# Kernel optimization log

Hardware: AMD Instinct MI355X
Metric: run time of the kernel (lower is better)

## Reference

```python
import jax, jax.numpy as jnp
import numpy as np

B, D = 64, 512          # batch, in_dims
P, PS, S = 128, 3, 64   # num_patches, patch_size, scene_size


def setup_inputs() -> dict:
    key = jax.random.key(0)
    k0, k1, k2, k3 = jax.random.split(key, 4)
    z = jax.random.normal(k0, (B, D), jnp.float32)
    Wm = jax.random.normal(k1, (P * PS * PS, D), jnp.float32) * 0.02
    bm = jnp.zeros((P * PS * PS,), jnp.float32)
    Wt = jax.random.normal(k2, (6 * P, D), jnp.float32) * 0.01
    # module initializes transform bias to [scale,0,0,0,scale,0] per patch (scale=2)
    bt = jnp.tile(jnp.array([2.0, 0.0, 0.0, 0.0, 2.0, 0.0], jnp.float32), P)
    noise = jax.random.normal(k3, (PS, PS), jnp.float32)
    return {"z": z, "Wm": Wm, "bm": bm, "Wt": Wt, "bt": bt, "noise": noise}


def _affine_grid(theta, size):
    # theta: (N,2,3). Matches torch affine_grid(align_corners=False).
    c = (jnp.arange(size, dtype=theta.dtype) + 0.5) / size * 2.0 - 1.0
    xg, yg = jnp.meshgrid(c, c)  # xg[h,w]=c[w], yg[h,w]=c[h]
    base = jnp.stack([xg, yg, jnp.ones_like(xg)], axis=-1)  # (S,S,3)
    return jnp.einsum('nij,hwj->nhwi', theta, base)  # (N,S,S,2), [...,0]=x, [...,1]=y


def _grid_sample_bilinear_zeros(img, grid):
    # img: (N,Hi,Wi), grid: (N,Ho,Wo,2). torch grid_sample bilinear, zeros padding,
    # align_corners=False.
    N, Hi, Wi = img.shape
    ix = ((grid[..., 0] + 1.0) * Wi - 1.0) * 0.5
    iy = ((grid[..., 1] + 1.0) * Hi - 1.0) * 0.5
    ix0 = jnp.floor(ix)
    iy0 = jnp.floor(iy)
    wx1 = ix - ix0
    wy1 = iy - iy0
    wx0 = 1.0 - wx1
    wy0 = 1.0 - wy1
    b = jnp.arange(N)[:, None, None]

    def gather(xf, yf):
        xi = xf.astype(jnp.int32)
        yi = yf.astype(jnp.int32)
        valid = (xi >= 0) & (xi < Wi) & (yi >= 0) & (yi < Hi)
        xc = jnp.clip(xi, 0, Wi - 1)
        yc = jnp.clip(yi, 0, Hi - 1)
        return jnp.where(valid, img[b, yc, xc], 0.0)

    v00 = gather(ix0, iy0)
    v01 = gather(ix0 + 1.0, iy0)
    v10 = gather(ix0, iy0 + 1.0)
    v11 = gather(ix0 + 1.0, iy0 + 1.0)
    return (wy0 * (wx0 * v00 + wx1 * v01) + wy1 * (wx0 * v10 + wx1 * v11))


def reference(z, Wm, bm, Wt, bt, noise):
    Bz = z.shape[0]
    # refine_patches=True path: masks = 1 - sigmoid(Linear(z))
    masks = 1.0 - jax.nn.sigmoid(z @ Wm.T + bm)
    masks = masks.reshape(Bz, P, PS, PS) * noise  # patch_noise multiply
    theta = (z @ Wt.T + bt).reshape(Bz, P, 2, 3)
    imgs = masks.reshape(Bz * P, PS, PS)
    th = theta.reshape(Bz * P, 2, 3)
    grid = _affine_grid(th, S)                      # (B*P, S, S, 2)
    out = _grid_sample_bilinear_zeros(imgs, grid)   # (B*P, S, S)
    return out.reshape(Bz, P, S, S)
```

## Files before the change

### kernel.cpp

```cpp
#include <hip/hip_runtime.h>
#include <math.h>

#define BATCH 64
#define DIM 512
#define NPATCH 128
#define SSZ 64
#define NMASK 1152
#define NTHETA 768
#define NROWS 1920

__global__ __launch_bounds__(256) void k1_gemm(
    const float* __restrict__ z, const float* __restrict__ Wm,
    const float* __restrict__ bm, const float* __restrict__ Wt,
    const float* __restrict__ bt, const float* __restrict__ noise,
    float* __restrict__ tmp) {
  __shared__ float zs[64][65];
  __shared__ float ws[16][64];

  const int t = threadIdx.x;
  const int rowBase = blockIdx.x * 16;
  const int b = t & 63;
  const int rgrp = t >> 6;

  float acc0 = 0.f, acc1 = 0.f, acc2 = 0.f, acc3 = 0.f;

  const int zb = t >> 2, zseg = t & 3;
  const int wrow = t >> 4, wseg = t & 15;
  const int j_w = rowBase + wrow;
  const float* wsrc = (j_w < NMASK) ? (Wm + (size_t)j_w * DIM)
                                    : (Wt + (size_t)(j_w - NMASK) * DIM);

  for (int kc = 0; kc < DIM; kc += 64) {
    __syncthreads();
    {
      const float4* zsrc4 = (const float4*)(z + (size_t)zb * DIM + kc + zseg * 16);
      float* zd = &zs[zb][zseg * 16];
#pragma unroll
      for (int u = 0; u < 4; ++u) {
        float4 a = zsrc4[u];
        zd[u * 4 + 0] = a.x; zd[u * 4 + 1] = a.y;
        zd[u * 4 + 2] = a.z; zd[u * 4 + 3] = a.w;
      }
    }
    {
      float4 wv = *(const float4*)(wsrc + kc + wseg * 4);
      *(float4*)&ws[wrow][wseg * 4] = wv;
    }
    __syncthreads();
#pragma unroll 8
    for (int k = 0; k < 64; ++k) {
      float zv = zs[b][k];
      acc0 = fmaf(zv, ws[rgrp * 4 + 0][k], acc0);
      acc1 = fmaf(zv, ws[rgrp * 4 + 1][k], acc1);
      acc2 = fmaf(zv, ws[rgrp * 4 + 2][k], acc2);
      acc3 = fmaf(zv, ws[rgrp * 4 + 3][k], acc3);
    }
  }

  float accs[4] = {acc0, acc1, acc2, acc3};
#pragma unroll
  for (int rr = 0; rr < 4; ++rr) {
    int j = rowBase + rgrp * 4 + rr;
    float v = accs[rr];
    if (j < NMASK) {
      v = 1.0f / (1.0f + expf(v + bm[j]));
      v *= noise[j % 9];
    } else {
      v += bt[j - NMASK];
    }
    tmp[(size_t)j * 64 + b] = v;
  }
}

__global__ __launch_bounds__(256) void k2_sample(
    const float* __restrict__ tmp, float* __restrict__ out) {
  __shared__ float msp[56];
  __shared__ float ths[6];

  const int t = threadIdx.x;
  const int bp = blockIdx.x;
  const int b = bp >> 7;
  const int p = bp & 127;

  if (t < 56) {
    int r = t >> 3, c = t & 7;
    float v = 0.0f;
    if (r >= 2 && r <= 4 && c >= 2 && c <= 4) {
      int q = (r - 2) * 3 + (c - 2);
      v = tmp[(size_t)(p * 9 + q) * 64 + b];
    }
    msp[t] = v;
  } else if (t < 62) {
    ths[t - 56] = tmp[(size_t)(NMASK + p * 6 + (t - 56)) * 64 + b];
  }
  __syncthreads();

  const float th0 = ths[0], th1 = ths[1], th2 = ths[2];
  const float th3 = ths[3], th4 = ths[4], th5 = ths[5];

  const int w = t & 63;
  const float cx = (w + 0.5f) * (1.0f / 32.0f) - 1.0f;
  const float A  = fmaf(1.5f, fmaf(th0, cx, th2), 1.0f);
  const float Bx = 1.5f * th1;
  const float C  = fmaf(1.5f, fmaf(th3, cx, th5), 1.0f);
  const float By = 1.5f * th4;

  float* obase = out + ((size_t)bp << 12) + t;
  const int h0 = t >> 6;

#pragma unroll
  for (int i = 0; i < 16; ++i) {
    const int h = h0 + i * 4;
    const float cy = (h + 0.5f) * (1.0f / 32.0f) - 1.0f;
    float ix = fmaf(Bx, cy, A);
    float iy = fmaf(By, cy, C);
    ix = fminf(fmaxf(ix, -1.5f), 3.5f);
    iy = fminf(fmaxf(iy, -1.5f), 3.5f);
    float fx0 = floorf(ix);
    float fy0 = floorf(iy);
    float fx = ix - fx0;
    float fy = iy - fy0;
    int xi = (int)fx0;
    int yi = (int)fy0;
    int idx = (yi + 2) * 8 + (xi + 2);
    float v00 = msp[idx];
    float v01 = msp[idx + 1];
    float v10 = msp[idx + 8];
    float v11 = msp[idx + 9];
    float wx0 = 1.0f - fx;
    float t0 = fmaf(fx, v01, wx0 * v00);
    float t1 = fmaf(fx, v11, wx0 * v10);
    float r  = fmaf(fy, t1, (1.0f - fy) * t0);
    obase[(size_t)i * 256] = r;
  }
}

extern "C" void kernel_launch(void* const* d_in, const int* in_sizes, int n_in,
                              void* d_out, int out_size, void* d_ws, size_t ws_size,
                              hipStream_t stream) {
  const float* z     = (const float*)d_in[0];
  const float* Wm    = (const float*)d_in[1];
  const float* bm    = (const float*)d_in[2];
  const float* Wt    = (const float*)d_in[3];
  const float* bt    = (const float*)d_in[4];
  const float* noise = (const float*)d_in[5];
  float* out = (float*)d_out;
  float* tmp = (float*)d_ws;

  hipLaunchKernelGGL(k1_gemm, dim3(NROWS / 16), dim3(256), 0, stream,
                     z, Wm, bm, Wt, bt, noise, tmp);
  hipLaunchKernelGGL(k2_sample, dim3(BATCH * NPATCH), dim3(256), 0, stream,
                     tmp, out);
}
```

Measured before the change: 164.2 us.

## Use tent-weight bilinear sampling with float4 stores in sample kernel

Replaces the floor-and-gather bilinear lookup from a padded shared-memory patch with a closed-form tent-weight sum over the nine patch values held in registers. Each thread now computes four adjacent output pixels incrementally and writes them with a single float4 store. The aim is to remove the dynamic LDS indexing, floor and int conversion, and to widen global stores. In exchange each pixel costs more ALU work (six weights and a 3x3 weighted sum), and the incremental coordinate updates may round slightly differently from the original.

```diff
diff --git a/kernel.cpp b/kernel.cpp
--- a/kernel.cpp
+++ b/kernel.cpp
@@ -74,64 +74,61 @@
 
 __global__ __launch_bounds__(256) void k2_sample(
     const float* __restrict__ tmp, float* __restrict__ out) {
-  __shared__ float msp[56];
-  __shared__ float ths[6];
+  __shared__ float sm[15];
 
   const int t = threadIdx.x;
   const int bp = blockIdx.x;
   const int b = bp >> 7;
   const int p = bp & 127;
 
-  if (t < 56) {
-    int r = t >> 3, c = t & 7;
-    float v = 0.0f;
-    if (r >= 2 && r <= 4 && c >= 2 && c <= 4) {
-      int q = (r - 2) * 3 + (c - 2);
-      v = tmp[(size_t)(p * 9 + q) * 64 + b];
-    }
-    msp[t] = v;
-  } else if (t < 62) {
-    ths[t - 56] = tmp[(size_t)(NMASK + p * 6 + (t - 56)) * 64 + b];
+  if (t < 9) {
+    sm[t] = tmp[(size_t)(p * 9 + t) * 64 + b];
+  } else if (t < 15) {
+    sm[t] = tmp[(size_t)(NMASK + p * 6 + (t - 9)) * 64 + b];
   }
   __syncthreads();
 
-  const float th0 = ths[0], th1 = ths[1], th2 = ths[2];
-  const float th3 = ths[3], th4 = ths[4], th5 = ths[5];
+  const float m00 = sm[0], m01 = sm[1], m02 = sm[2];
+  const float m10 = sm[3], m11 = sm[4], m12 = sm[5];
+  const float m20 = sm[6], m21 = sm[7], m22 = sm[8];
+  const float th0 = sm[9], th1 = sm[10], th2 = sm[11];
+  const float th3 = sm[12], th4 = sm[13], th5 = sm[14];
 
-  const int w = t & 63;
-  const float cx = (w + 0.5f) * (1.0f / 32.0f) - 1.0f;
-  const float A  = fmaf(1.5f, fmaf(th0, cx, th2), 1.0f);
-  const float Bx = 1.5f * th1;
-  const float C  = fmaf(1.5f, fmaf(th3, cx, th5), 1.0f);
-  const float By = 1.5f * th4;
+  const int w4 = (t & 15) << 2;
+  const int hb = t >> 4;
+  const float cx0 = (w4 + 0.5f) * (1.0f / 32.0f) - 1.0f;
+  const float cy0 = (hb + 0.5f) * (1.0f / 32.0f) - 1.0f;
+  const float dix = th0 * (1.5f / 32.0f);
+  const float diy = th3 * (1.5f / 32.0f);
+  const float Bx = 1.5f * th1, By = 1.5f * th4;
+  const float Px = fmaf(1.5f, fmaf(th0, cx0, th2), 1.0f);
+  const float Py = fmaf(1.5f, fmaf(th3, cx0, th5), 1.0f);
 
-  float* obase = out + ((size_t)bp << 12) + t;
-  const int h0 = t >> 6;
+  float* op = out + ((size_t)bp << 12) + hb * 64 + w4;
 
 #pragma unroll
-  for (int i = 0; i < 16; ++i) {
-    const int h = h0 + i * 4;
-    const float cy = (h + 0.5f) * (1.0f / 32.0f) - 1.0f;
-    float ix = fmaf(Bx, cy, A);
-    float iy = fmaf(By, cy, C);
-    ix = fminf(fmaxf(ix, -1.5f), 3.5f);
-    iy = fminf(fmaxf(iy, -1.5f), 3.5f);
-    float fx0 = floorf(ix);
-    float fy0 = floorf(iy);
-    float fx = ix - fx0;
-    float fy = iy - fy0;
-    int xi = (int)fx0;
-    int yi = (int)fy0;
-    int idx = (yi + 2) * 8 + (xi + 2);
-    float v00 = msp[idx];
-    float v01 = msp[idx + 1];
-    float v10 = msp[idx + 8];
-    float v11 = msp[idx + 9];
-    float wx0 = 1.0f - fx;
-    float t0 = fmaf(fx, v01, wx0 * v00);
-    float t1 = fmaf(fx, v11, wx0 * v10);
-    float r  = fmaf(fy, t1, (1.0f - fy) * t0);
-    obase[(size_t)i * 256] = r;
+  for (int i = 0; i < 4; ++i) {
+    const float cy = cy0 + 0.5f * i;
+    float ix = fmaf(Bx, cy, Px);
+    float iy = fmaf(By, cy, Py);
+    float4 r;
+    float* rp = &r.x;
+#pragma unroll
+    for (int j = 0; j < 4; ++j) {
+      const float wx0 = fmaxf(1.0f - fabsf(ix), 0.0f);
+      const float wx1 = fmaxf(1.0f - fabsf(ix - 1.0f), 0.0f);
+      const float wx2 = fmaxf(1.0f - fabsf(ix - 2.0f), 0.0f);
+      const float wy0 = fmaxf(1.0f - fabsf(iy), 0.0f);
+      const float wy1 = fmaxf(1.0f - fabsf(iy - 1.0f), 0.0f);
+      const float wy2 = fmaxf(1.0f - fabsf(iy - 2.0f), 0.0f);
+      const float s0 = fmaf(m02, wx2, fmaf(m01, wx1, m00 * wx0));
+      const float s1 = fmaf(m12, wx2, fmaf(m11, wx1, m10 * wx0));
+      const float s2 = fmaf(m22, wx2, fmaf(m21, wx1, m20 * wx0));
+      rp[j] = fmaf(wy2, s2, fmaf(wy1, s1, wy0 * s0));
+      ix += dix;
+      iy += diy;
+    }
+    *(float4*)(op + i * 16 * 64) = r;
   }
 }
 
```

After: 162.5 us. About the same (-1.0%).
